# Optimization experiments

Hardware: AMD Instinct MI355X
Metric: run time of the kernel (lower is better)

Reference implementation:

```python
import jax, jax.numpy as jnp
import numpy as np

B = 1048576
VEC_SZ = 4
LUT_BITS = 8
K = 2 ** LUT_BITS  # 256 codewords


def setup_inputs() -> dict:
    key = jax.random.key(0)
    kx, kt = jax.random.split(key)
    X = jax.random.normal(kx, (B, VEC_SZ), dtype=jnp.float32)
    tlut = jax.random.normal(kt, (K, VEC_SZ), dtype=jnp.float32)  # codebook [K, vec_sz]
    return {"X": X, "tlut": tlut}


def reference(X, tlut):
    # torch.cdist(X, tlut) -> argmin is equivalent to argmin of squared distances:
    x_sq = jnp.sum(X * X, axis=-1, keepdims=True)            # [B, 1]
    c_sq = jnp.sum(tlut * tlut, axis=-1)                     # [K]
    cross = jnp.einsum('bd,kd->bk', X, tlut)                 # [B, K]
    dist2 = x_sq - 2.0 * cross + c_sq                        # [B, K]
    state = jnp.argmin(dist2, axis=-1).astype(jnp.int32)     # [B]
    hatX = jnp.take(tlut, state, axis=0)                     # gather reconstruction [B, vec_sz]
    return hatX, state
```

## Files before the change

### kernel.cpp

```cpp
#include <hip/hip_runtime.h>

typedef float f32x2 __attribute__((ext_vector_type(2)));

#define K_CW 256
#define NJ (K_CW / 2)
#define PPT 2

struct PK2 { f32x2 c0, c1, c2, c3, cs, pad; };

__device__ __forceinline__ f32x2 pk_mul_vs(f32x2 a, f32x2 b) {
    f32x2 d; asm("v_pk_mul_f32 %0, %1, %2" : "=v"(d) : "v"(a), "s"(b)); return d;
}
__device__ __forceinline__ f32x2 pk_fma_vsv(f32x2 a, f32x2 b, f32x2 c) {
    f32x2 d; asm("v_pk_fma_f32 %0, %1, %2, %3" : "=v"(d) : "v"(a), "s"(b), "v"(c)); return d;
}
__device__ __forceinline__ f32x2 pk_fma_vvv(f32x2 a, f32x2 b, f32x2 c) {
    f32x2 d; asm("v_pk_fma_f32 %0, %1, %2, %3" : "=v"(d) : "v"(a), "v"(b), "v"(c)); return d;
}
__device__ __forceinline__ f32x2 pk_add_vs(f32x2 a, f32x2 b) {
    f32x2 d; asm("v_pk_add_f32 %0, %1, %2" : "=v"(d) : "v"(a), "s"(b)); return d;
}

__global__ void vq_pack_kernel(const float* __restrict__ tlut, float* __restrict__ pk) {
    int k = threadIdx.x;
    float c0 = tlut[k * 4 + 0];
    float c1 = tlut[k * 4 + 1];
    float c2 = tlut[k * 4 + 2];
    float c3 = tlut[k * 4 + 3];
    float s = __fadd_rn(__fadd_rn(__fadd_rn(__fmul_rn(c0, c0), __fmul_rn(c1, c1)),
                                  __fmul_rn(c2, c2)),
                        __fmul_rn(c3, c3));
    const int j = k >> 1, o = k & 1;
    float* e = pk + j * 12;
    e[0 + o] = c0; e[2 + o] = c1; e[4 + o] = c2; e[6 + o] = c3; e[8 + o] = s;
    if (o == 0) { e[10] = 0.f; e[11] = 0.f; }
}

__global__ __launch_bounds__(256, 8) void vq_argmin_kernel(
    const float* __restrict__ X,
    const float* __restrict__ tlut,
    const float* __restrict__ pk,
    float* __restrict__ outX,
    float* __restrict__ outS,
    int B) {
    const int g = blockIdx.x * 256 + threadIdx.x;
    const int stride = B / PPT;

    const float4* __restrict__ X4 = reinterpret_cast<const float4*>(X);
    const float4* __restrict__ T4 = reinterpret_cast<const float4*>(tlut);
    const PK2* __restrict__ PKB = reinterpret_cast<const PK2*>(pk);

    f32x2 xb0[PPT], xb1[PPT], xb2[PPT], xb3[PPT], xsqb[PPT];
    float bestd[PPT];
    int besti[PPT];

    #pragma unroll
    for (int i = 0; i < PPT; ++i) {
        const float4 xv = X4[g + i * stride];
        const float xsq =
            __fadd_rn(__fadd_rn(__fadd_rn(__fmul_rn(xv.x, xv.x), __fmul_rn(xv.y, xv.y)),
                                __fmul_rn(xv.z, xv.z)),
                      __fmul_rn(xv.w, xv.w));
        xb0[i] = f32x2{xv.x, xv.x};
        xb1[i] = f32x2{xv.y, xv.y};
        xb2[i] = f32x2{xv.z, xv.z};
        xb3[i] = f32x2{xv.w, xv.w};
        xsqb[i] = f32x2{xsq, xsq};
        bestd[i] = __builtin_inff();
        besti[i] = 0;
    }
    const f32x2 m2 = f32x2{-2.0f, -2.0f};

    #pragma unroll 16
    for (int j = 0; j < NJ; ++j) {
        const PK2 e = PKB[j];
        const int k0 = j * 2;
        #pragma unroll
        for (int i = 0; i < PPT; ++i) {
            f32x2 cr = pk_mul_vs(xb0[i], e.c0);
            cr = pk_fma_vsv(xb1[i], e.c1, cr);
            cr = pk_fma_vsv(xb2[i], e.c2, cr);
            cr = pk_fma_vsv(xb3[i], e.c3, cr);
            const f32x2 t2 = pk_fma_vvv(m2, cr, xsqb[i]);
            const f32x2 d = pk_add_vs(t2, e.cs);
            besti[i] = (d[0] < bestd[i]) ? k0 : besti[i];
            bestd[i] = fminf(d[0], bestd[i]);
            besti[i] = (d[1] < bestd[i]) ? (k0 + 1) : besti[i];
            bestd[i] = fminf(d[1], bestd[i]);
        }
    }

    #pragma unroll
    for (int i = 0; i < PPT; ++i) {
        const int p = g + i * stride;
        reinterpret_cast<float4*>(outX)[p] = T4[besti[i]];
        outS[p] = (float)besti[i];
    }
}

extern "C" void kernel_launch(void* const* d_in, const int* in_sizes, int n_in,
                              void* d_out, int out_size, void* d_ws, size_t ws_size,
                              hipStream_t stream) {
    const float* X    = (const float*)d_in[0];
    const float* tlut = (const float*)d_in[1];
    const int B = in_sizes[0] / 4;

    float* outX = (float*)d_out;
    float* outS = outX + (size_t)B * 4;

    float* pk = (float*)d_ws;

    vq_pack_kernel<<<1, 256, 0, stream>>>(tlut, pk);

    const int groups = B / PPT;
    const int grid = groups / 256;
    vq_argmin_kernel<<<grid, 256, 0, stream>>>(X, tlut, pk, outX, outS, B);
}
```

Before: 140.7 us.

## Build packed codebook in LDS per block instead of separate pack kernel

```diff
diff --git a/kernel.cpp b/kernel.cpp
--- a/kernel.cpp
+++ b/kernel.cpp
@@ -6,49 +6,43 @@
 #define NJ (K_CW / 2)
 #define PPT 2
 
-struct PK2 { f32x2 c0, c1, c2, c3, cs, pad; };
-
-__device__ __forceinline__ f32x2 pk_mul_vs(f32x2 a, f32x2 b) {
-    f32x2 d; asm("v_pk_mul_f32 %0, %1, %2" : "=v"(d) : "v"(a), "s"(b)); return d;
+__device__ __forceinline__ f32x2 pk_mul(f32x2 a, f32x2 b) {
+    f32x2 d; asm("v_pk_mul_f32 %0, %1, %2" : "=v"(d) : "v"(a), "v"(b)); return d;
 }
-__device__ __forceinline__ f32x2 pk_fma_vsv(f32x2 a, f32x2 b, f32x2 c) {
-    f32x2 d; asm("v_pk_fma_f32 %0, %1, %2, %3" : "=v"(d) : "v"(a), "s"(b), "v"(c)); return d;
-}
-__device__ __forceinline__ f32x2 pk_fma_vvv(f32x2 a, f32x2 b, f32x2 c) {
+__device__ __forceinline__ f32x2 pk_fma(f32x2 a, f32x2 b, f32x2 c) {
     f32x2 d; asm("v_pk_fma_f32 %0, %1, %2, %3" : "=v"(d) : "v"(a), "v"(b), "v"(c)); return d;
 }
-__device__ __forceinline__ f32x2 pk_add_vs(f32x2 a, f32x2 b) {
-    f32x2 d; asm("v_pk_add_f32 %0, %1, %2" : "=v"(d) : "v"(a), "s"(b)); return d;
-}
-
-__global__ void vq_pack_kernel(const float* __restrict__ tlut, float* __restrict__ pk) {
-    int k = threadIdx.x;
-    float c0 = tlut[k * 4 + 0];
-    float c1 = tlut[k * 4 + 1];
-    float c2 = tlut[k * 4 + 2];
-    float c3 = tlut[k * 4 + 3];
-    float s = __fadd_rn(__fadd_rn(__fadd_rn(__fmul_rn(c0, c0), __fmul_rn(c1, c1)),
-                                  __fmul_rn(c2, c2)),
-                        __fmul_rn(c3, c3));
-    const int j = k >> 1, o = k & 1;
-    float* e = pk + j * 12;
-    e[0 + o] = c0; e[2 + o] = c1; e[4 + o] = c2; e[6 + o] = c3; e[8 + o] = s;
-    if (o == 0) { e[10] = 0.f; e[11] = 0.f; }
+__device__ __forceinline__ f32x2 pk_add(f32x2 a, f32x2 b) {
+    f32x2 d; asm("v_pk_add_f32 %0, %1, %2" : "=v"(d) : "v"(a), "v"(b)); return d;
 }
 
 __global__ __launch_bounds__(256, 8) void vq_argmin_kernel(
     const float* __restrict__ X,
     const float* __restrict__ tlut,
-    const float* __restrict__ pk,
     float* __restrict__ outX,
     float* __restrict__ outS,
     int B) {
-    const int g = blockIdx.x * 256 + threadIdx.x;
+    __shared__ f32x2 scb[NJ * 6];
+
+    const int t = threadIdx.x;
+    const int g = blockIdx.x * 256 + t;
     const int stride = B / PPT;
 
     const float4* __restrict__ X4 = reinterpret_cast<const float4*>(X);
     const float4* __restrict__ T4 = reinterpret_cast<const float4*>(tlut);
-    const PK2* __restrict__ PKB = reinterpret_cast<const PK2*>(pk);
+
+    {
+        const float4 cv = T4[t];
+        const float s = __fadd_rn(__fadd_rn(__fadd_rn(__fmul_rn(cv.x, cv.x),
+                                                      __fmul_rn(cv.y, cv.y)),
+                                            __fmul_rn(cv.z, cv.z)),
+                                  __fmul_rn(cv.w, cv.w));
+        const int j = t >> 1, o = t & 1;
+        float* e = reinterpret_cast<float*>(&scb[j * 6]);
+        e[0 + o] = cv.x; e[2 + o] = cv.y; e[4 + o] = cv.z; e[6 + o] = cv.w;
+        e[8 + o] = s;
+        if (o == 0) { e[10] = 0.f; e[11] = 0.f; }
+    }
 
     f32x2 xb0[PPT], xb1[PPT], xb2[PPT], xb3[PPT], xsqb[PPT];
     float bestd[PPT];
@@ -71,18 +65,24 @@
     }
     const f32x2 m2 = f32x2{-2.0f, -2.0f};
 
-    #pragma unroll 16
+    __syncthreads();
+
+    #pragma unroll 8
     for (int j = 0; j < NJ; ++j) {
-        const PK2 e = PKB[j];
+        const f32x2 c0p = scb[j * 6 + 0];
+        const f32x2 c1p = scb[j * 6 + 1];
+        const f32x2 c2p = scb[j * 6 + 2];
+        const f32x2 c3p = scb[j * 6 + 3];
+        const f32x2 csp = scb[j * 6 + 4];
         const int k0 = j * 2;
         #pragma unroll
         for (int i = 0; i < PPT; ++i) {
-            f32x2 cr = pk_mul_vs(xb0[i], e.c0);
-            cr = pk_fma_vsv(xb1[i], e.c1, cr);
-            cr = pk_fma_vsv(xb2[i], e.c2, cr);
-            cr = pk_fma_vsv(xb3[i], e.c3, cr);
-            const f32x2 t2 = pk_fma_vvv(m2, cr, xsqb[i]);
-            const f32x2 d = pk_add_vs(t2, e.cs);
+            f32x2 cr = pk_mul(xb0[i], c0p);
+            cr = pk_fma(xb1[i], c1p, cr);
+            cr = pk_fma(xb2[i], c2p, cr);
+            cr = pk_fma(xb3[i], c3p, cr);
+            const f32x2 t2 = pk_fma(m2, cr, xsqb[i]);
+            const f32x2 d = pk_add(t2, csp);
             besti[i] = (d[0] < bestd[i]) ? k0 : besti[i];
             bestd[i] = fminf(d[0], bestd[i]);
             besti[i] = (d[1] < bestd[i]) ? (k0 + 1) : besti[i];
@@ -108,11 +108,7 @@
     float* outX = (float*)d_out;
     float* outS = outX + (size_t)B * 4;
 
-    float* pk = (float*)d_ws;
-
-    vq_pack_kernel<<<1, 256, 0, stream>>>(tlut, pk);
-
     const int groups = B / PPT;
     const int grid = groups / 256;
-    vq_argmin_kernel<<<grid, 256, 0, stream>>>(X, tlut, pk, outX, outS, B);
+    vq_argmin_kernel<<<grid, 256, 0, stream>>>(X, tlut, outX, outS, B);
 }
```

Result: faster. 129.3 us (-8.1%).
